# Performance work log

Hardware: AMD Instinct MI355X
Metric: run time of the kernel (lower is better)

Reference implementation:

```python
import math
import jax, jax.numpy as jnp
import numpy as np

B, T, C, H = 2, 2048, 1024, 16
D = C // H


def _slopes(n):
    def p2(m):
        start = 2 ** (-(2 ** -(math.log2(m) - 3)))
        return [start * start ** i for i in range(m)]
    if math.log2(n).is_integer():
        return p2(n)
    c = 2 ** math.floor(math.log2(n))
    return p2(c) + _slopes(2 * c)[0::2][: n - c]


def setup_inputs() -> dict:
    key = jax.random.key(0)
    ks = jax.random.split(key, 9)
    std = 0.02
    x = jax.random.normal(ks[0], (B, T, C), dtype=jnp.float32)
    Wq = std * jax.random.normal(ks[1], (C, C), dtype=jnp.float32)
    Wk = std * jax.random.normal(ks[2], (C, C), dtype=jnp.float32)
    Wv = std * jax.random.normal(ks[3], (C, C), dtype=jnp.float32)
    # fc_resid init: std 0.02/sqrt(num_layers)
    Wo = (std / math.sqrt(24.0)) * jax.random.normal(ks[4], (C, C), dtype=jnp.float32)
    bq = jnp.zeros((C,), jnp.float32)
    bk = jnp.zeros((C,), jnp.float32)
    bv = jnp.zeros((C,), jnp.float32)
    bo = jnp.zeros((C,), jnp.float32)
    return {"x": x, "Wq": Wq, "bq": bq, "Wk": Wk, "bk": bk,
            "Wv": Wv, "bv": bv, "Wo": Wo, "bo": bo}


def reference(x, Wq, bq, Wk, bk, Wv, bv, Wo, bo):
    # projections -> [B, T, H, D]
    q = (x @ Wq + bq).reshape(B, T, H, D)
    k = (x @ Wk + bk).reshape(B, T, H, D)
    v = (x @ Wv + bv).reshape(B, T, H, D)

    scale = 1.0 / math.sqrt(D)
    att = jnp.einsum("bqhd,bkhd->bhqk", q, k) * scale  # [B,H,T,T]

    slopes = jnp.asarray(_slopes(H), dtype=jnp.float32)  # [H]
    i = jnp.arange(T)
    rel = i[None, :] - i[None, :].T  # rel[i,j] = j - i
    causal = rel <= 0  # j <= i
    # alibi bias: -tril(i - j) = tril(j - i), scaled per head
    alibi = slopes[:, None, None] * jnp.where(causal, rel, 0).astype(jnp.float32)

    att = att + alibi[None]  # broadcast over batch
    att = jnp.where(causal[None, None], att, -jnp.inf)
    att = jax.nn.softmax(att, axis=-1)

    y = jnp.einsum("bhqk,bkhd->bqhd", att, v).reshape(B, T, C)
    return y @ Wo + bo  # dropout p=0 (eval) is identity
```

## Files before the change

### kernel.cpp

```cpp
#include <hip/hip_runtime.h>
#include <hip/hip_bf16.h>

typedef __bf16 bf16;
typedef __bf16 bf16x4 __attribute__((ext_vector_type(4)));
typedef __bf16 bf16x8 __attribute__((ext_vector_type(8)));
typedef float floatx4 __attribute__((ext_vector_type(4)));
typedef short short4_ __attribute__((ext_vector_type(4)));

#define B_ 2
#define T_ 2048
#define C_ 1024
#define H_ 16
#define D_ 64
#define M_ 4096
#define QK_LD 2048

__device__ __forceinline__ void load_lds16(const void* g, void* l) {
  __builtin_amdgcn_global_load_lds(
      (const __attribute__((address_space(1))) unsigned int*)g,
      (__attribute__((address_space(3))) unsigned int*)l, 16, 0, 0);
}

__device__ __forceinline__ floatx4 mfma16(bf16x4 a, bf16x4 b, floatx4 c) {
#if __has_builtin(__builtin_amdgcn_mfma_f32_16x16x16_bf16)
  return __builtin_amdgcn_mfma_f32_16x16x16_bf16(a, b, c, 0, 0, 0);
#else
  return __builtin_amdgcn_mfma_f32_16x16x16bf16_1k(
      __builtin_bit_cast(short4_, a), __builtin_bit_cast(short4_, b), c, 0, 0, 0);
#endif
}

__device__ __forceinline__ bf16x4 lo4(bf16x8 v) {
  return __builtin_shufflevector(v, v, 0, 1, 2, 3);
}
__device__ __forceinline__ bf16x4 hi4(bf16x8 v) {
  return __builtin_shufflevector(v, v, 4, 5, 6, 7);
}

struct PrepArgs { const float* w[4]; bf16* wt[4]; const float* x; bf16* xb; };

__global__ __launch_bounds__(256)
void prep(PrepArgs p) {
  const int bid = blockIdx.x;
  if (bid < 4096) {
    __shared__ float tile[32][33];
    const int z = bid >> 10, xy = bid & 1023;
    const int bx = xy & 31, by = xy >> 5;
    const float* in = p.w[z];
    bf16* out = p.wt[z];
    int tx = threadIdx.x & 31, ty = threadIdx.x >> 5;
    int n0 = bx * 32, k0 = by * 32;
#pragma unroll
    for (int j = 0; j < 32; j += 8)
      tile[ty + j][tx] = in[(size_t)(k0 + ty + j) * C_ + n0 + tx];
    __syncthreads();
#pragma unroll
    for (int j = 0; j < 32; j += 8)
      out[(size_t)(n0 + ty + j) * C_ + k0 + tx] = (bf16)tile[tx][ty + j];
  } else {
    int i = ((bid - 4096) * 256 + threadIdx.x) * 8;
    float4 a = *(const float4*)(p.x + i);
    float4 b = *(const float4*)(p.x + i + 4);
    bf16x8 o;
    o[0] = (bf16)a.x; o[1] = (bf16)a.y; o[2] = (bf16)a.z; o[3] = (bf16)a.w;
    o[4] = (bf16)b.x; o[5] = (bf16)b.y; o[6] = (bf16)b.z; o[7] = (bf16)b.w;
    *(bf16x8*)(p.xb + i) = o;
  }
}

struct GQ {
  const bf16* A; const bf16* Bt;
  const float* bias[3];
  bf16* Cout; bf16* vt; int N; int K;
};

__global__ __launch_bounds__(256, 2)
void gemm128(GQ g) {
  __shared__ __align__(16) bf16 As[128 * 64];
  __shared__ __align__(16) bf16 Bs[128 * 64];
  const int tid = threadIdx.x;
  const int wave = tid >> 6, lane = tid & 63;
  const int quad = lane >> 4, l16 = lane & 15;
  const int m0 = blockIdx.y * 128, n0 = blockIdx.x * 128;
  const int wm = (wave >> 1) * 64, wn = (wave & 1) * 64;

  floatx4 acc[4][4] = {};

  int rA[4], cA[4];
#pragma unroll
  for (int t = 0; t < 4; ++t) {
    int pch = (wave * 4 + t) * 64 + lane;
    rA[t] = pch >> 3;
    cA[t] = (pch & 7) ^ (rA[t] & 7);
  }

  for (int k0 = 0; k0 < g.K; k0 += 64) {
    __syncthreads();
#pragma unroll
    for (int t = 0; t < 4; ++t) {
      load_lds16(g.A + (size_t)(m0 + rA[t]) * g.K + k0 + cA[t] * 8,
                 As + (wave * 4 + t) * 512);
      load_lds16(g.Bt + (size_t)(n0 + rA[t]) * g.K + k0 + cA[t] * 8,
                 Bs + (wave * 4 + t) * 512);
    }
    __builtin_amdgcn_s_waitcnt(0x0f70);
    __syncthreads();
#pragma unroll
    for (int s = 0; s < 2; ++s) {
      bf16x8 af[4], bfr[4];
#pragma unroll
      for (int i = 0; i < 4; ++i) {
        int mr = wm + i * 16 + l16;
        af[i] = *(const bf16x8*)(As + ((mr * 8) + ((s * 4 + quad) ^ (mr & 7))) * 8);
        int nr = wn + i * 16 + l16;
        bfr[i] = *(const bf16x8*)(Bs + ((nr * 8) + ((s * 4 + quad) ^ (nr & 7))) * 8);
      }
#pragma unroll
      for (int i = 0; i < 4; ++i)
#pragma unroll
        for (int j = 0; j < 4; ++j)
          acc[i][j] = __builtin_amdgcn_mfma_f32_16x16x32_bf16(af[i], bfr[j],
                                                              acc[i][j], 0, 0, 0);
    }
  }

  const bool vsplit = (n0 >= 2048);
#pragma unroll
  for (int j = 0; j < 4; ++j) {
    int col = n0 + wn + j * 16 + l16;
    const float* bp = g.bias[col >> 10];
    float bv = bp[col & 1023];
    if (vsplit) {
      int cv = col - 2048;
      bf16* dstb = g.vt + ((size_t)((m0 >> 11) * 16 + (cv >> 6)) * 64 + (cv & 63)) * (size_t)T_
                   + (m0 & 2047) + wm + quad * 8;
#pragma unroll
      for (int ii = 0; ii < 2; ++ii) {
        bf16x8 pk;
#pragma unroll
        for (int r = 0; r < 8; ++r)
          pk[r] = (bf16)(acc[ii * 2 + (r >> 2)][j][r & 3] + bv);
        *(bf16x8*)(dstb + ii * 32) = pk;
      }
    } else {
#pragma unroll
      for (int i = 0; i < 4; ++i) {
#pragma unroll
        for (int r = 0; r < 4; ++r) {
          int row = m0 + wm + i * 16 + quad * 4 + r;
          g.Cout[(size_t)row * g.N + col] = (bf16)(acc[i][j][r] + bv);
        }
      }
    }
  }
}

__global__ __launch_bounds__(256, 2)
void gemm_out(const bf16* __restrict__ A, const bf16* __restrict__ Bt,
              const float* __restrict__ bias, float* __restrict__ C) {
  __shared__ __align__(16) bf16 As[64 * 64];
  __shared__ __align__(16) bf16 Bs[128 * 64];
  const int tid = threadIdx.x;
  const int wave = tid >> 6, lane = tid & 63;
  const int quad = lane >> 4, l16 = lane & 15;
  const int m0 = blockIdx.y * 64, n0 = blockIdx.x * 128;
  const int wm = (wave >> 1) * 32, wn = (wave & 1) * 64;

  floatx4 acc[2][4] = {};

  int rA[2], cA[2], rB[4], cB[4];
#pragma unroll
  for (int t = 0; t < 2; ++t) {
    int p = t * 256 + tid;
    rA[t] = p >> 3; cA[t] = (p & 7) ^ (rA[t] & 7);
  }
#pragma unroll
  for (int t = 0; t < 4; ++t) {
    int p = t * 256 + tid;
    rB[t] = p >> 3; cB[t] = (p & 7) ^ (rB[t] & 7);
  }

  for (int k0 = 0; k0 < 1024; k0 += 64) {
    __syncthreads();
#pragma unroll
    for (int t = 0; t < 2; ++t)
      load_lds16(A + (size_t)(m0 + rA[t]) * 1024 + k0 + cA[t] * 8,
                 As + t * 2048 + wave * 512);
#pragma unroll
    for (int t = 0; t < 4; ++t)
      load_lds16(Bt + (size_t)(n0 + rB[t]) * 1024 + k0 + cB[t] * 8,
                 Bs + t * 2048 + wave * 512);
    __builtin_amdgcn_s_waitcnt(0x0f70);
    __syncthreads();
#pragma unroll
    for (int s = 0; s < 2; ++s) {
      bf16x8 af[2], bfr[4];
#pragma unroll
      for (int i = 0; i < 2; ++i) {
        int mr = wm + i * 16 + l16;
        af[i] = *(const bf16x8*)(As + ((mr * 8) + ((s * 4 + quad) ^ (mr & 7))) * 8);
      }
#pragma unroll
      for (int j = 0; j < 4; ++j) {
        int nr = wn + j * 16 + l16;
        bfr[j] = *(const bf16x8*)(Bs + ((nr * 8) + ((s * 4 + quad) ^ (nr & 7))) * 8);
      }
#pragma unroll
      for (int i = 0; i < 2; ++i)
#pragma unroll
        for (int j = 0; j < 4; ++j)
          acc[i][j] = __builtin_amdgcn_mfma_f32_16x16x32_bf16(af[i], bfr[j],
                                                              acc[i][j], 0, 0, 0);
    }
  }

#pragma unroll
  for (int j = 0; j < 4; ++j) {
    int col = n0 + wn + j * 16 + l16;
    float bv = bias[col];
#pragma unroll
    for (int i = 0; i < 2; ++i)
#pragma unroll
      for (int r = 0; r < 4; ++r) {
        int row = m0 + wm + i * 16 + quad * 4 + r;
        C[(size_t)row * 1024 + col] = acc[i][j][r] + bv;
      }
  }
}

__global__ __launch_bounds__(512, 2)
void attn8(const bf16* __restrict__ qk, const bf16* __restrict__ vt,
           bf16* __restrict__ y, bf16* __restrict__ po, float* __restrict__ pl) {
  __shared__ __align__(16) bf16 smem[32768];
  const int tid = threadIdx.x, wave = tid >> 6, lane = tid & 63;
  const int quad = lane >> 4, l16 = lane & 15;
  const int qs = wave >> 1, kh = wave & 1;
  const int id = blockIdx.x;
  const int bh = (id & 7) * 4 + ((id >> 3) & 3);
  const int rem = id >> 5;
  const int p = rem >> 1;
  const bool roleB = rem & 1;
  const int b = bh >> 4, h = bh & 15;

  const float L2E = 1.4426950408889634f;
  const float slope2 = exp2f(-0.5f * (float)(h + 1)) * L2E;
  const float scl2 = 0.125f * L2E;
  const float M0 = 14.0f;

  const int rS = tid >> 3;
  const int cS = (tid & 7) ^ (rS & 7);
  const bf16* kbase = qk + (size_t)b * T_ * QK_LD + 1024 + h * 64;
  const bf16* vbase = vt + (size_t)bh * 64 * T_;

  float kc[2][4];
#pragma unroll
  for (int kt = 0; kt < 2; ++kt)
#pragma unroll
    for (int r = 0; r < 4; ++r)
      kc[kt][r] = slope2 * (float)(kt * 16 + quad * 4 + r);

  int qb_ = roleB ? (15 - p) : p;
  int t0_ = 0;
  int t1_ = roleB ? 17 : (2 * p + 2);
  int sg_ = roleB ? 0 : -1;

  for (int ph = 0;; ++ph) {
    const int w0 = qb_ * 128 + qs * 32;
    const int qi0 = w0 + l16;
    float qoff[2];
    qoff[0] = slope2 * (float)qi0 + M0;
    qoff[1] = qoff[0] + slope2 * 16.0f;

    bf16x8 qf[2][2];
#pragma unroll
    for (int qt = 0; qt < 2; ++qt)
#pragma unroll
      for (int s = 0; s < 2; ++s)
        qf[qt][s] = *(const bf16x8*)(qk +
            (size_t)(b * T_ + w0 + qt * 16 + l16) * QK_LD + h * 64 + s * 32 + quad * 8);

    floatx4 o[2][4];
#pragma unroll
    for (int qt = 0; qt < 2; ++qt)
#pragma unroll
      for (int n = 0; n < 4; ++n) o[qt][n] = (floatx4)0.f;
    floatx4 lsv[2];
    lsv[0] = (floatx4)0.f; lsv[1] = (floatx4)0.f;

    auto tilebody = [&](const bf16* Klc, const bf16* Vlc, int t) {
      const int kj0 = t * 64;
      bf16x8 kf[2][2];
#pragma unroll
      for (int ss = 0; ss < 2; ++ss)
#pragma unroll
        for (int kt = 0; kt < 2; ++kt) {
          const int krow = kh * 32 + kt * 16 + l16;
          kf[ss][kt] = *(const bf16x8*)(Klc + krow * 64 +
                                        (((ss * 4 + quad) ^ (krow & 7)) * 8));
        }
      bf16x8 vf8[4];
#pragma unroll
      for (int nt = 0; nt < 4; ++nt) {
        const int drow = nt * 16 + l16;
        vf8[nt] = *(const bf16x8*)(Vlc + drow * 64 +
                                   (((kh * 4 + quad) ^ (drow & 7)) * 8));
      }

      const int kbi = kj0 + kh * 32;
      const float kb = slope2 * (float)kbi;

      __builtin_amdgcn_s_setprio(1);
#pragma unroll
      for (int qt = 0; qt < 2; ++qt) {
        const int rb = w0 + qt * 16;
        floatx4 st[2] = {};
#pragma unroll
        for (int ss = 0; ss < 2; ++ss)
#pragma unroll
          for (int kt = 0; kt < 2; ++kt)
            st[kt] = __builtin_amdgcn_mfma_f32_16x16x32_bf16(kf[ss][kt], qf[qt][ss],
                                                             st[kt], 0, 0, 0);

        const float bb = kb - qoff[qt];
        const int qi = qi0 + qt * 16;
        bf16x4 pb[2];
        if (kbi + 31 > rb) {
#pragma unroll
          for (int kt = 0; kt < 2; ++kt) {
#pragma unroll
            for (int r = 0; r < 4; ++r) {
              float pv = __builtin_amdgcn_exp2f(
                  fmaf(st[kt][r], scl2, bb + kc[kt][r]));
              if (kbi + kt * 16 + quad * 4 + r > qi) pv = 0.f;
              lsv[qt][r] += pv;
              pb[kt][r] = (bf16)pv;
            }
          }
        } else {
#pragma unroll
          for (int kt = 0; kt < 2; ++kt) {
#pragma unroll
            for (int r = 0; r < 4; ++r) {
              float pv = __builtin_amdgcn_exp2f(
                  fmaf(st[kt][r], scl2, bb + kc[kt][r]));
              lsv[qt][r] += pv;
              pb[kt][r] = (bf16)pv;
            }
          }
        }

#pragma unroll
        for (int nt = 0; nt < 4; ++nt) {
          o[qt][nt] = mfma16(lo4(vf8[nt]), pb[0], o[qt][nt]);
          o[qt][nt] = mfma16(hi4(vf8[nt]), pb[1], o[qt][nt]);
        }
      }
      __builtin_amdgcn_s_setprio(0);
    };

#pragma unroll
    for (int s2 = 0; s2 < 2; ++s2) {
      load_lds16(kbase + (size_t)((t0_ + s2) * 64 + rS) * QK_LD + cS * 8,
                 smem + s2 * 4096 + wave * 512);
      load_lds16(vbase + (size_t)rS * T_ + (t0_ + s2) * 64 + cS * 8,
                 smem + 16384 + s2 * 4096 + wave * 512);
    }
    __builtin_amdgcn_s_waitcnt(0x0f70);
    __syncthreads();

    const int len = t1_ - t0_;
    const int npair = len >> 1;
    const int nit = (len + 1) >> 1;
    for (int it = 0; it < npair; ++it) {
      const int cur = it & 1;
      if (it + 1 < nit) {
        const int nt0 = t0_ + 2 * it + 2;
#pragma unroll
        for (int s2 = 0; s2 < 2; ++s2) {
          load_lds16(kbase + (size_t)((nt0 + s2) * 64 + rS) * QK_LD + cS * 8,
                     smem + (cur ^ 1) * 8192 + s2 * 4096 + wave * 512);
          load_lds16(vbase + (size_t)rS * T_ + (nt0 + s2) * 64 + cS * 8,
                     smem + 16384 + (cur ^ 1) * 8192 + s2 * 4096 + wave * 512);
        }
      }
      tilebody(smem + cur * 8192,        smem + 16384 + cur * 8192,        t0_ + 2 * it);
      tilebody(smem + cur * 8192 + 4096, smem + 16384 + cur * 8192 + 4096, t0_ + 2 * it + 1);
      __builtin_amdgcn_s_waitcnt(0x0f70);
      __syncthreads();
    }
    if (len & 1) {
      const int cur = npair & 1;
      tilebody(smem + cur * 8192, smem + 16384 + cur * 8192, t1_ - 1);
      __syncthreads();
    }

    float* Cb = (float*)smem;
    float lsum[2];
#pragma unroll
    for (int qt = 0; qt < 2; ++qt)
      lsum[qt] = (lsv[qt][0] + lsv[qt][1]) + (lsv[qt][2] + lsv[qt][3]);
    if (kh == 1) {
#pragma unroll
      for (int qt = 0; qt < 2; ++qt) {
#pragma unroll
        for (int n = 0; n < 4; ++n)
          *(floatx4*)(Cb + (((qs * 2 + qt) * 4 + n) * 64 + lane) * 4) = o[qt][n];
        Cb[8192 + (qs * 2 + qt) * 64 + lane] = lsum[qt];
      }
    }
    __syncthreads();
    if (kh == 0) {
#pragma unroll
      for (int qt = 0; qt < 2; ++qt) {
#pragma unroll
        for (int n = 0; n < 4; ++n)
          o[qt][n] += *(const floatx4*)(Cb + (((qs * 2 + qt) * 4 + n) * 64 + lane) * 4);
        lsum[qt] += Cb[8192 + (qs * 2 + qt) * 64 + lane];
        lsum[qt] += __shfl_xor(lsum[qt], 16);
        lsum[qt] += __shfl_xor(lsum[qt], 32);
      }

      if (sg_ < 0) {
#pragma unroll
        for (int qt = 0; qt < 2; ++qt) {
          const float inv = 1.f / lsum[qt];
          bf16* yp = y + (size_t)(b * T_ + w0 + qt * 16 + l16) * C_ + h * 64 + quad * 4;
#pragma unroll
          for (int nt = 0; nt < 4; ++nt) {
            bf16x4 pk;
#pragma unroll
            for (int r = 0; r < 4; ++r) pk[r] = (bf16)(o[qt][nt][r] * inv);
            *(bf16x4*)(yp + nt * 16) = pk;
          }
        }
      } else {
        const int pid = (bh * 8 + (qb_ - 8)) * 2 + sg_;
        bf16* pob = po + (size_t)pid * 8192;
#pragma unroll
        for (int qt = 0; qt < 2; ++qt) {
#pragma unroll
          for (int half = 0; half < 2; ++half) {
            bf16x8 pk;
#pragma unroll
            for (int jj = 0; jj < 8; ++jj)
              pk[jj] = (bf16)o[qt][half * 2 + (jj >> 2)][jj & 3];
            *(bf16x8*)(pob + (qt * 2 + half) * 2048 + (qs * 64 + lane) * 8) = pk;
          }
          if (quad == 0)
            pl[pid * 128 + qs * 32 + qt * 16 + l16] = lsum[qt];
        }
      }
    }
    __syncthreads();

    if (roleB || ph == 1) break;
    qb_ = 15 - p; t0_ = 17; t1_ = 32 - 2 * p; sg_ = 1;
  }
}

__global__ __launch_bounds__(256)
void combine(const bf16* __restrict__ po, const float* __restrict__ pl,
             bf16* __restrict__ y) {
  const int x = blockIdx.x;
  const int bh = x >> 3, qb = (x & 7) + 8;
  const int b = bh >> 4, h = bh & 15;
  const int pid0 = (bh * 8 + (qb - 8)) * 2;
  const bf16* p0 = po + (size_t)pid0 * 8192;
  const bf16* p1 = p0 + 8192;
  const int t = threadIdx.x;
  const int qs = t >> 6, quad = (t >> 4) & 3, l16 = t & 15;

  float linv[2];
  int row[2];
#pragma unroll
  for (int qt = 0; qt < 2; ++qt) {
    row[qt] = qs * 32 + qt * 16 + l16;
    linv[qt] = 1.f / (pl[pid0 * 128 + row[qt]] + pl[(pid0 + 1) * 128 + row[qt]]);
  }

#pragma unroll
  for (int qt = 0; qt < 2; ++qt)
#pragma unroll
    for (int half = 0; half < 2; ++half) {
      bf16x8 a = *(const bf16x8*)(p0 + (qt * 2 + half) * 2048 + t * 8);
      bf16x8 c = *(const bf16x8*)(p1 + (qt * 2 + half) * 2048 + t * 8);
#pragma unroll
      for (int g = 0; g < 2; ++g) {
        bf16x4 outv;
#pragma unroll
        for (int r = 0; r < 4; ++r)
          outv[r] = (bf16)(((float)a[g * 4 + r] + (float)c[g * 4 + r]) * linv[qt]);
        const int col = (half * 2 + g) * 16 + quad * 4;
        *(bf16x4*)(y + (size_t)(b * T_ + qb * 128 + row[qt]) * C_ + h * 64 + col) = outv;
      }
    }
}

extern "C" void kernel_launch(void* const* d_in, const int* in_sizes, int n_in,
                              void* d_out, int out_size, void* d_ws, size_t ws_size,
                              hipStream_t stream) {
  const float* x  = (const float*)d_in[0];
  const float* Wq = (const float*)d_in[1];
  const float* bq = (const float*)d_in[2];
  const float* Wk = (const float*)d_in[3];
  const float* bk = (const float*)d_in[4];
  const float* Wv = (const float*)d_in[5];
  const float* bv = (const float*)d_in[6];
  const float* Wo = (const float*)d_in[7];
  const float* bo = (const float*)d_in[8];

  bf16* ws  = (bf16*)d_ws;
  bf16* WtQ = ws;
  bf16* WtK = WtQ + (size_t)C_ * C_;
  bf16* WtV = WtK + (size_t)C_ * C_;
  bf16* WtO = WtV + (size_t)C_ * C_;
  bf16* xb  = WtO + (size_t)C_ * C_;
  bf16* qkb = xb + (size_t)M_ * C_;
  bf16* vtb = qkb + (size_t)M_ * 2 * C_;
  bf16* yb  = vtb + (size_t)M_ * C_;
  bf16* pob = yb + (size_t)M_ * C_;
  float* plb = (float*)(pob + (size_t)512 * 8192);

  PrepArgs pp;
  pp.w[0] = Wq; pp.w[1] = Wk; pp.w[2] = Wv; pp.w[3] = Wo;
  pp.wt[0] = WtQ; pp.wt[1] = WtK; pp.wt[2] = WtV; pp.wt[3] = WtO;
  pp.x = x; pp.xb = xb;
  prep<<<dim3(4096 + M_ * C_ / (256 * 8)), 256, 0, stream>>>(pp);

  GQ gq;
  gq.A = xb; gq.Bt = WtQ;
  gq.bias[0] = bq; gq.bias[1] = bk; gq.bias[2] = bv;
  gq.Cout = qkb; gq.vt = vtb; gq.N = 2 * C_; gq.K = C_;
  gemm128<<<dim3(24, 32), 256, 0, stream>>>(gq);

  attn8<<<dim3(512), 512, 0, stream>>>(qkb, vtb, yb, pob, plb);
  combine<<<dim3(32 * 8), 256, 0, stream>>>(pob, plb, yb);

  gemm_out<<<dim3(8, 64), 256, 0, stream>>>(yb, WtO, bo, (float*)d_out);
}
```

Baseline: 178.8 us.

## Replace paired double-buffered K/V tiles with a three-stage single-tile ring

The attention loop used to load two K/V tiles at a time into double buffers and sync once per pair. It now uses a three-slot ring of single tiles, prefetching two tiles ahead. Partial vmcnt waits (0x0f72) let the next loads stay in flight across the barrier. This shrinks LDS from 64KB to 48KB and aims to hide load latency better. The cost is one barrier per tile instead of one per pair.

```diff
diff --git a/kernel.cpp b/kernel.cpp
--- a/kernel.cpp
+++ b/kernel.cpp
@@ -231,7 +231,7 @@
 __global__ __launch_bounds__(512, 2)
 void attn8(const bf16* __restrict__ qk, const bf16* __restrict__ vt,
            bf16* __restrict__ y, bf16* __restrict__ po, float* __restrict__ pl) {
-  __shared__ __align__(16) bf16 smem[32768];
+  __shared__ __align__(16) bf16 smem[24576];
   const int tid = threadIdx.x, wave = tid >> 6, lane = tid & 63;
   const int quad = lane >> 4, l16 = lane & 15;
   const int qs = wave >> 1, kh = wave & 1;
@@ -363,36 +363,38 @@
       load_lds16(kbase + (size_t)((t0_ + s2) * 64 + rS) * QK_LD + cS * 8,
                  smem + s2 * 4096 + wave * 512);
       load_lds16(vbase + (size_t)rS * T_ + (t0_ + s2) * 64 + cS * 8,
-                 smem + 16384 + s2 * 4096 + wave * 512);
-    }
-    __builtin_amdgcn_s_waitcnt(0x0f70);
-    __syncthreads();
+                 smem + 12288 + s2 * 4096 + wave * 512);
+    }
+    __builtin_amdgcn_s_waitcnt(0x0f72);
+    __builtin_amdgcn_sched_barrier(0);
+    __builtin_amdgcn_s_barrier();
+    __builtin_amdgcn_sched_barrier(0);
 
     const int len = t1_ - t0_;
-    const int npair = len >> 1;
-    const int nit = (len + 1) >> 1;
-    for (int it = 0; it < npair; ++it) {
-      const int cur = it & 1;
-      if (it + 1 < nit) {
-        const int nt0 = t0_ + 2 * it + 2;
-#pragma unroll
-        for (int s2 = 0; s2 < 2; ++s2) {
-          load_lds16(kbase + (size_t)((nt0 + s2) * 64 + rS) * QK_LD + cS * 8,
-                     smem + (cur ^ 1) * 8192 + s2 * 4096 + wave * 512);
-          load_lds16(vbase + (size_t)rS * T_ + (nt0 + s2) * 64 + cS * 8,
-                     smem + 16384 + (cur ^ 1) * 8192 + s2 * 4096 + wave * 512);
-        }
-      }
-      tilebody(smem + cur * 8192,        smem + 16384 + cur * 8192,        t0_ + 2 * it);
-      tilebody(smem + cur * 8192 + 4096, smem + 16384 + cur * 8192 + 4096, t0_ + 2 * it + 1);
-      __builtin_amdgcn_s_waitcnt(0x0f70);
-      __syncthreads();
-    }
-    if (len & 1) {
-      const int cur = npair & 1;
-      tilebody(smem + cur * 8192, smem + 16384 + cur * 8192, t1_ - 1);
-      __syncthreads();
-    }
+    int cur = 0;
+    for (int it = 0; it < len; ++it) {
+      const bool morestage = (it + 2 < len);
+      if (morestage) {
+        const int nt = t0_ + it + 2;
+        const int nb = (cur + 2 >= 3) ? cur - 1 : cur + 2;
+        load_lds16(kbase + (size_t)(nt * 64 + rS) * QK_LD + cS * 8,
+                   smem + nb * 4096 + wave * 512);
+        load_lds16(vbase + (size_t)rS * T_ + nt * 64 + cS * 8,
+                   smem + 12288 + nb * 4096 + wave * 512);
+      }
+
+      tilebody(smem + cur * 4096, smem + 12288 + cur * 4096, t0_ + it);
+
+      if (it + 1 < len) {
+        if (morestage) __builtin_amdgcn_s_waitcnt(0x0f72);
+        else           __builtin_amdgcn_s_waitcnt(0x0f70);
+        __builtin_amdgcn_sched_barrier(0);
+        __builtin_amdgcn_s_barrier();
+        __builtin_amdgcn_sched_barrier(0);
+      }
+      cur = (cur + 1 >= 3) ? 0 : cur + 1;
+    }
+    __syncthreads();
 
     float* Cb = (float*)smem;
     float lsum[2];
```

After: 180.1 us. Within noise of the previous version (+0.7%).

## Compute softmax row sums via MFMA with ones and remap GEMM blocks per XCD

Applied to the files above, without the earlier changes.

The attention kernel stops accumulating softmax denominators with per-element VALU adds. Instead it runs two extra MFMAs per tile that multiply a ones vector by the bf16 probabilities, which also removes the final cross-lane shuffle reduction. The row sum now comes from bf16-rounded probabilities, so it matches what the PV product uses, at the cost of extra matrix-core work. Both GEMMs move to 1D grids with explicit block-to-tile mapping; the QKV GEMM groups N tiles by XCD (id&7) to improve L2 locality of the weight columns.

```diff
diff --git a/kernel.cpp b/kernel.cpp
--- a/kernel.cpp
+++ b/kernel.cpp
@@ -81,7 +81,10 @@
   const int tid = threadIdx.x;
   const int wave = tid >> 6, lane = tid & 63;
   const int quad = lane >> 4, l16 = lane & 15;
-  const int m0 = blockIdx.y * 128, n0 = blockIdx.x * 128;
+  const int id = blockIdx.x;
+  const int xcd = id & 7, pos = id >> 3;
+  const int mI = pos / 3, nl = pos - mI * 3;
+  const int m0 = mI * 128, n0 = (xcd * 3 + nl) * 128;
   const int wm = (wave >> 1) * 64, wn = (wave & 1) * 64;
 
   floatx4 acc[4][4] = {};
@@ -163,7 +166,8 @@
   const int tid = threadIdx.x;
   const int wave = tid >> 6, lane = tid & 63;
   const int quad = lane >> 4, l16 = lane & 15;
-  const int m0 = blockIdx.y * 64, n0 = blockIdx.x * 128;
+  const int id = blockIdx.x;
+  const int m0 = (id >> 3) * 64, n0 = (id & 7) * 128;
   const int wm = (wave >> 1) * 32, wn = (wave & 1) * 64;
 
   floatx4 acc[2][4] = {};
@@ -247,6 +251,10 @@
   const float scl2 = 0.125f * L2E;
   const float M0 = 14.0f;
 
+  bf16x4 onesA;
+#pragma unroll
+  for (int j = 0; j < 4; ++j) onesA[j] = (bf16)1.0f;
+
   const int rS = tid >> 3;
   const int cS = (tid & 7) ^ (rS & 7);
   const bf16* kbase = qk + (size_t)b * T_ * QK_LD + 1024 + h * 64;
@@ -284,8 +292,8 @@
     for (int qt = 0; qt < 2; ++qt)
 #pragma unroll
       for (int n = 0; n < 4; ++n) o[qt][n] = (floatx4)0.f;
-    floatx4 lsv[2];
-    lsv[0] = (floatx4)0.f; lsv[1] = (floatx4)0.f;
+    floatx4 lacc[2];
+    lacc[0] = (floatx4)0.f; lacc[1] = (floatx4)0.f;
 
     auto tilebody = [&](const bf16* Klc, const bf16* Vlc, int t) {
       const int kj0 = t * 64;
@@ -332,7 +340,6 @@
               float pv = __builtin_amdgcn_exp2f(
                   fmaf(st[kt][r], scl2, bb + kc[kt][r]));
               if (kbi + kt * 16 + quad * 4 + r > qi) pv = 0.f;
-              lsv[qt][r] += pv;
               pb[kt][r] = (bf16)pv;
             }
           }
@@ -340,14 +347,14 @@
 #pragma unroll
           for (int kt = 0; kt < 2; ++kt) {
 #pragma unroll
-            for (int r = 0; r < 4; ++r) {
-              float pv = __builtin_amdgcn_exp2f(
+            for (int r = 0; r < 4; ++r)
+              pb[kt][r] = (bf16)__builtin_amdgcn_exp2f(
                   fmaf(st[kt][r], scl2, bb + kc[kt][r]));
-              lsv[qt][r] += pv;
-              pb[kt][r] = (bf16)pv;
-            }
           }
         }
+
+        lacc[qt] = mfma16(onesA, pb[0], lacc[qt]);
+        lacc[qt] = mfma16(onesA, pb[1], lacc[qt]);
 
 #pragma unroll
         for (int nt = 0; nt < 4; ++nt) {
@@ -397,8 +404,7 @@
     float* Cb = (float*)smem;
     float lsum[2];
 #pragma unroll
-    for (int qt = 0; qt < 2; ++qt)
-      lsum[qt] = (lsv[qt][0] + lsv[qt][1]) + (lsv[qt][2] + lsv[qt][3]);
+    for (int qt = 0; qt < 2; ++qt) lsum[qt] = lacc[qt][0];
     if (kh == 1) {
 #pragma unroll
       for (int qt = 0; qt < 2; ++qt) {
@@ -416,8 +422,6 @@
         for (int n = 0; n < 4; ++n)
           o[qt][n] += *(const floatx4*)(Cb + (((qs * 2 + qt) * 4 + n) * 64 + lane) * 4);
         lsum[qt] += Cb[8192 + (qs * 2 + qt) * 64 + lane];
-        lsum[qt] += __shfl_xor(lsum[qt], 16);
-        lsum[qt] += __shfl_xor(lsum[qt], 32);
       }
 
       if (sg_ < 0) {
@@ -531,10 +535,10 @@
   gq.A = xb; gq.Bt = WtQ;
   gq.bias[0] = bq; gq.bias[1] = bk; gq.bias[2] = bv;
   gq.Cout = qkb; gq.vt = vtb; gq.N = 2 * C_; gq.K = C_;
-  gemm128<<<dim3(24, 32), 256, 0, stream>>>(gq);
+  gemm128<<<dim3(768), 256, 0, stream>>>(gq);
 
   attn8<<<dim3(512), 512, 0, stream>>>(qkb, vtb, yb, pob, plb);
   combine<<<dim3(32 * 8), 256, 0, stream>>>(pob, plb, yb);
 
-  gemm_out<<<dim3(8, 64), 256, 0, stream>>>(yb, WtO, bo, (float*)d_out);
-}
+  gemm_out<<<dim3(512), 256, 0, stream>>>(yb, WtO, bo, (float*)d_out);
+}
```

Result: no change. 180.1 us (median of 2 runs) (+0.7%).
